# Kernel optimization log

Hardware: AMD Instinct MI355X
Metric: run time of the kernel (lower is better)

## Reference

```python
import jax, jax.numpy as jnp
import numpy as np

S, NB, C = 7, 2, 20
LAMBDA_COORD, LAMBDA_NOOBJ = 5.0, 0.5
EPS = 1e-6


def _iou(a, b):
    """Midpoint-format IoU. a, b: [..., 4] = (x, y, w, h)."""
    ax1, ay1 = a[..., 0] - a[..., 2] / 2, a[..., 1] - a[..., 3] / 2
    ax2, ay2 = a[..., 0] + a[..., 2] / 2, a[..., 1] + a[..., 3] / 2
    bx1, by1 = b[..., 0] - b[..., 2] / 2, b[..., 1] - b[..., 3] / 2
    bx2, by2 = b[..., 0] + b[..., 2] / 2, b[..., 1] + b[..., 3] / 2
    iw = jnp.clip(jnp.minimum(ax2, bx2) - jnp.maximum(ax1, bx1), 0.0)
    ih = jnp.clip(jnp.minimum(ay2, by2) - jnp.maximum(ay1, by1), 0.0)
    inter = iw * ih
    area_a = jnp.abs((ax2 - ax1) * (ay2 - ay1))
    area_b = jnp.abs((bx2 - bx1) * (by2 - by1))
    return inter / (area_a + area_b - inter + EPS)


def setup_inputs() -> dict:
    key = jax.random.key(0)
    k1, k2, k3, k4 = jax.random.split(key, 4)
    N = 16384
    predictions = jax.random.uniform(k1, (N, S * S * (C + NB * 5)), dtype=jnp.float32)
    cls = jax.random.uniform(k2, (N, S, S, C), dtype=jnp.float32)
    box_rest = jax.random.uniform(k3, (N, S, S, 4), dtype=jnp.float32)  # y,w,h,conf
    u = jax.random.uniform(k4, (N, S, S, 2), dtype=jnp.float32)
    flag = jnp.where(u[..., 0] < 0.3, 1.0, u[..., 1] * 0.99)
    targets = jnp.concatenate([cls, flag[..., None], box_rest], axis=-1)  # [N,S,S,25]
    return {"predictions": predictions, "targets": targets}


def reference(predictions, targets):
    N = predictions.shape[0]
    pred = predictions.reshape(N, S, S, C + NB * 5)
    class_pred = pred[..., :C]                      # [N,S,S,20]
    b1 = pred[..., C:C + 5]                         # [N,S,S,5]
    b2 = pred[..., C + 5:C + 10]                    # [N,S,S,5]
    tbox = targets[..., C:C + 5]                    # [N,S,S,5]
    obj = (targets[..., C] == 1.0).astype(pred.dtype)  # [N,S,S]

    iou1 = _iou(b1[..., :4], tbox[..., :4])
    iou2 = _iou(b2[..., :4], tbox[..., :4])
    resp = jnp.where((iou1 > iou2)[..., None], b1, b2)  # responsible box [N,S,S,5]

    xy = (resp[..., 0] - tbox[..., 0]) ** 2 + (resp[..., 1] - tbox[..., 1]) ** 2
    wh = (jnp.sqrt(resp[..., 2]) - jnp.sqrt(tbox[..., 2])) ** 2 \
       + (jnp.sqrt(resp[..., 3]) - jnp.sqrt(tbox[..., 3])) ** 2
    coord = LAMBDA_COORD * (xy + wh)
    conf = (resp[..., 4] - tbox[..., 4]) ** 2
    cls_loss = jnp.sum((class_pred - targets[..., :C]) ** 2, axis=-1)

    obj_terms = jnp.sum(obj * (coord + conf + cls_loss))
    noobj_terms = LAMBDA_NOOBJ * jnp.sum((1.0 - obj) * (b1[..., 4] ** 2 + b2[..., 4] ** 2))
    return (obj_terms + noobj_terms) / N
```

## Files before the change

### kernel.cpp

```cpp
#include <hip/hip_runtime.h>
#include <math.h>

#define SS 7
#define CC 20
#define CELL_PRED 30
#define CELL_TGT  25
#define BLOCK 64

__device__ __forceinline__ float iou_box(const float* __restrict__ a,
                                         const float* __restrict__ b) {
    const float EPS = 1e-6f;
    float ax1 = a[0] - a[2] * 0.5f, ay1 = a[1] - a[3] * 0.5f;
    float ax2 = a[0] + a[2] * 0.5f, ay2 = a[1] + a[3] * 0.5f;
    float bx1 = b[0] - b[2] * 0.5f, by1 = b[1] - b[3] * 0.5f;
    float bx2 = b[0] + b[2] * 0.5f, by2 = b[1] + b[3] * 0.5f;
    float iw = fmaxf(fminf(ax2, bx2) - fmaxf(ax1, bx1), 0.0f);
    float ih = fmaxf(fminf(ay2, by2) - fmaxf(ay1, by1), 0.0f);
    float inter = iw * ih;
    float area_a = fabsf((ax2 - ax1) * (ay2 - ay1));
    float area_b = fabsf((bx2 - bx1) * (by2 - by1));
    return inter / (area_a + area_b - inter + EPS);
}

__global__ __launch_bounds__(BLOCK) void yolo_cell_loss(
    const float* __restrict__ pred,
    const float* __restrict__ tgt,
    float* __restrict__ partials,
    int nCells)
{
    __shared__ __align__(16) float s_pred[BLOCK * CELL_PRED];
    __shared__ __align__(16) float s_tgt [BLOCK * CELL_TGT];

    const int tid = threadIdx.x;
    const int blockCell = blockIdx.x * BLOCK;
    const bool fullBlock = (blockCell + BLOCK) <= nCells;

    if (fullBlock) {
        const float4* gp = (const float4*)(pred + (size_t)blockCell * CELL_PRED);
        float4* sp = (float4*)s_pred;
        #pragma unroll
        for (int i = tid; i < BLOCK * CELL_PRED / 4; i += BLOCK) sp[i] = gp[i];
        const float4* gt = (const float4*)(tgt + (size_t)blockCell * CELL_TGT);
        float4* st = (float4*)s_tgt;
        #pragma unroll
        for (int i = tid; i < BLOCK * CELL_TGT / 4; i += BLOCK) st[i] = gt[i];
    } else {
        int nc = nCells - blockCell;
        if (nc < 0) nc = 0;
        for (int i = tid; i < nc * CELL_PRED; i += BLOCK)
            s_pred[i] = pred[(size_t)blockCell * CELL_PRED + i];
        for (int i = tid; i < nc * CELL_TGT; i += BLOCK)
            s_tgt[i] = tgt[(size_t)blockCell * CELL_TGT + i];
    }
    __syncthreads();

    float loss = 0.0f;
    const int cell = blockCell + tid;
    if (cell < nCells) {
        const float* p = s_pred + tid * CELL_PRED;
        const float* t = s_tgt  + tid * CELL_TGT;

        const float* b1 = p + CC;
        const float* b2 = p + CC + 5;
        const float* tb = t + CC;

        float obj = (tb[0] == 1.0f) ? 1.0f : 0.0f;

        float iou1 = iou_box(b1, tb);
        float iou2 = iou_box(b2, tb);
        bool pick1 = iou1 > iou2;
        float r0 = pick1 ? b1[0] : b2[0];
        float r1 = pick1 ? b1[1] : b2[1];
        float r2 = pick1 ? b1[2] : b2[2];
        float r3 = pick1 ? b1[3] : b2[3];
        float r4 = pick1 ? b1[4] : b2[4];

        float dx = r0 - tb[0], dy = r1 - tb[1];
        float xy = dx * dx + dy * dy;
        float dw = sqrtf(r2) - sqrtf(tb[2]);
        float dh = sqrtf(r3) - sqrtf(tb[3]);
        float wh = dw * dw + dh * dh;
        float coord = 5.0f * (xy + wh);
        float dconf = r4 - tb[4];
        float conf = dconf * dconf;

        float cls = 0.0f;
        #pragma unroll
        for (int k = 0; k < CC; ++k) {
            float d = p[k] - t[k];
            cls += d * d;
        }

        float noobj = 0.5f * (1.0f - obj) * (b1[4] * b1[4] + b2[4] * b2[4]);
        loss = obj * (coord + conf + cls) + noobj;
    }

    #pragma unroll
    for (int off = 32; off > 0; off >>= 1)
        loss += __shfl_down(loss, off, 64);
    if (tid == 0) partials[blockIdx.x] = loss;
}

__global__ __launch_bounds__(256) void yolo_final_reduce(
    const float* __restrict__ partials, int nPartials, double invN,
    float* __restrict__ out)
{
    __shared__ double s_red[4];
    double sum = 0.0;
    const float4* p4 = (const float4*)partials;
    int n4 = nPartials >> 2;
    for (int i = threadIdx.x; i < n4; i += 256) {
        float4 v = p4[i];
        sum += (double)v.x + (double)v.y + (double)v.z + (double)v.w;
    }
    for (int i = (n4 << 2) + threadIdx.x; i < nPartials; i += 256)
        sum += (double)partials[i];
    #pragma unroll
    for (int off = 32; off > 0; off >>= 1)
        sum += __shfl_down(sum, off, 64);
    if ((threadIdx.x & 63) == 0) s_red[threadIdx.x >> 6] = sum;
    __syncthreads();
    if (threadIdx.x == 0) {
        double s = s_red[0] + s_red[1] + s_red[2] + s_red[3];
        out[0] = (float)(s * invN);
    }
}

extern "C" void kernel_launch(void* const* d_in, const int* in_sizes, int n_in,
                              void* d_out, int out_size, void* d_ws, size_t ws_size,
                              hipStream_t stream) {
    const float* pred = (const float*)d_in[0];
    const float* tgt  = (const float*)d_in[1];
    float* out = (float*)d_out;
    float* partials = (float*)d_ws;

    const int N = in_sizes[0] / (SS * SS * CELL_PRED);
    const int nCells = N * SS * SS;
    const int nBlocks = (nCells + BLOCK - 1) / BLOCK;

    yolo_cell_loss<<<nBlocks, BLOCK, 0, stream>>>(pred, tgt, partials, nCells);
    yolo_final_reduce<<<1, 256, 0, stream>>>(partials, nBlocks, 1.0 / (double)N, out);
}
```

Measured before the change: 207.2 us.

## Replace shared-memory staging with grid-stride direct per-thread loads

Drops the LDS staging of each block's cells. Each thread now reads its own cell's prediction (as float2) and target values straight from global memory inside a grid-stride loop over a fixed grid of 1024 blocks of 256 threads, with a two-level shuffle plus shared-memory block reduction. This removes the __syncthreads barrier and LDS traffic and cuts the partials array to 1024 entries. The cost is uncoalesced strided per-thread loads (120-byte and 100-byte strides), which lean on the cache to merge accesses and may use bandwidth less efficiently than the old coalesced float4 staging.

```diff
diff --git a/kernel.cpp b/kernel.cpp
--- a/kernel.cpp
+++ b/kernel.cpp
@@ -5,115 +5,118 @@
 #define CC 20
 #define CELL_PRED 30
 #define CELL_TGT  25
-#define BLOCK 64
+#define BLOCK 256
+#define GRID 1024
 
-__device__ __forceinline__ float iou_box(const float* __restrict__ a,
-                                         const float* __restrict__ b) {
+__device__ __forceinline__ float cell_loss(const float* __restrict__ pred,
+                                           const float* __restrict__ tgt,
+                                           int c) {
     const float EPS = 1e-6f;
-    float ax1 = a[0] - a[2] * 0.5f, ay1 = a[1] - a[3] * 0.5f;
-    float ax2 = a[0] + a[2] * 0.5f, ay2 = a[1] + a[3] * 0.5f;
-    float bx1 = b[0] - b[2] * 0.5f, by1 = b[1] - b[3] * 0.5f;
-    float bx2 = b[0] + b[2] * 0.5f, by2 = b[1] + b[3] * 0.5f;
-    float iw = fmaxf(fminf(ax2, bx2) - fmaxf(ax1, bx1), 0.0f);
-    float ih = fmaxf(fminf(ay2, by2) - fmaxf(ay1, by1), 0.0f);
-    float inter = iw * ih;
-    float area_a = fabsf((ax2 - ax1) * (ay2 - ay1));
-    float area_b = fabsf((bx2 - bx1) * (by2 - by1));
-    return inter / (area_a + area_b - inter + EPS);
+    const float* tp = tgt + (size_t)c * CELL_TGT;
+    float tv[CELL_TGT];
+    #pragma unroll
+    for (int j = 0; j < CELL_TGT; ++j) tv[j] = tp[j];
+
+    const float2* p2 = (const float2*)(pred + (size_t)c * CELL_PRED);
+    float cls = 0.0f;
+    #pragma unroll
+    for (int j = 0; j < 10; ++j) {
+        float2 v = p2[j];
+        float d0 = v.x - tv[2 * j];
+        float d1 = v.y - tv[2 * j + 1];
+        cls += d0 * d0;
+        cls += d1 * d1;
+    }
+    float b[10];
+    #pragma unroll
+    for (int j = 0; j < 5; ++j) {
+        float2 v = p2[10 + j];
+        b[2 * j] = v.x; b[2 * j + 1] = v.y;
+    }
+    const float* b1 = b;
+    const float* b2 = b + 5;
+    const float* tb = tv + CC;
+
+    float obj = (tb[0] == 1.0f) ? 1.0f : 0.0f;
+
+    float t_x1 = tb[0] - tb[2] * 0.5f, t_y1 = tb[1] - tb[3] * 0.5f;
+    float t_x2 = tb[0] + tb[2] * 0.5f, t_y2 = tb[1] + tb[3] * 0.5f;
+    float t_area = fabsf((t_x2 - t_x1) * (t_y2 - t_y1));
+
+    float a_x1 = b1[0] - b1[2] * 0.5f, a_y1 = b1[1] - b1[3] * 0.5f;
+    float a_x2 = b1[0] + b1[2] * 0.5f, a_y2 = b1[1] + b1[3] * 0.5f;
+    float iw1 = fmaxf(fminf(a_x2, t_x2) - fmaxf(a_x1, t_x1), 0.0f);
+    float ih1 = fmaxf(fminf(a_y2, t_y2) - fmaxf(a_y1, t_y1), 0.0f);
+    float inter1 = iw1 * ih1;
+    float area1 = fabsf((a_x2 - a_x1) * (a_y2 - a_y1));
+    float iou1 = inter1 / (area1 + t_area - inter1 + EPS);
+
+    float c_x1 = b2[0] - b2[2] * 0.5f, c_y1 = b2[1] - b2[3] * 0.5f;
+    float c_x2 = b2[0] + b2[2] * 0.5f, c_y2 = b2[1] + b2[3] * 0.5f;
+    float iw2 = fmaxf(fminf(c_x2, t_x2) - fmaxf(c_x1, t_x1), 0.0f);
+    float ih2 = fmaxf(fminf(c_y2, t_y2) - fmaxf(c_y1, t_y1), 0.0f);
+    float inter2 = iw2 * ih2;
+    float area2 = fabsf((c_x2 - c_x1) * (c_y2 - c_y1));
+    float iou2 = inter2 / (area2 + t_area - inter2 + EPS);
+
+    bool pick1 = iou1 > iou2;
+    float r0 = pick1 ? b1[0] : b2[0];
+    float r1 = pick1 ? b1[1] : b2[1];
+    float r2 = pick1 ? b1[2] : b2[2];
+    float r3 = pick1 ? b1[3] : b2[3];
+    float r4 = pick1 ? b1[4] : b2[4];
+
+    float dx = r0 - tb[0], dy = r1 - tb[1];
+    float xy = dx * dx + dy * dy;
+    float dw = sqrtf(r2) - sqrtf(tb[2]);
+    float dh = sqrtf(r3) - sqrtf(tb[3]);
+    float wh = dw * dw + dh * dh;
+    float coord = 5.0f * (xy + wh);
+    float dconf = r4 - tb[4];
+    float conf = dconf * dconf;
+
+    float noobj = 0.5f * (1.0f - obj) * (b1[4] * b1[4] + b2[4] * b2[4]);
+    return obj * (coord + conf + cls) + noobj;
 }
 
-__global__ __launch_bounds__(BLOCK) void yolo_cell_loss(
+__global__ __launch_bounds__(BLOCK) void yolo_stream(
     const float* __restrict__ pred,
     const float* __restrict__ tgt,
     float* __restrict__ partials,
-    int nCells)
+    int nCells, int fullIters)
 {
-    __shared__ __align__(16) float s_pred[BLOCK * CELL_PRED];
-    __shared__ __align__(16) float s_tgt [BLOCK * CELL_TGT];
-
     const int tid = threadIdx.x;
-    const int blockCell = blockIdx.x * BLOCK;
-    const bool fullBlock = (blockCell + BLOCK) <= nCells;
-
-    if (fullBlock) {
-        const float4* gp = (const float4*)(pred + (size_t)blockCell * CELL_PRED);
-        float4* sp = (float4*)s_pred;
-        #pragma unroll
-        for (int i = tid; i < BLOCK * CELL_PRED / 4; i += BLOCK) sp[i] = gp[i];
-        const float4* gt = (const float4*)(tgt + (size_t)blockCell * CELL_TGT);
-        float4* st = (float4*)s_tgt;
-        #pragma unroll
-        for (int i = tid; i < BLOCK * CELL_TGT / 4; i += BLOCK) st[i] = gt[i];
-    } else {
-        int nc = nCells - blockCell;
-        if (nc < 0) nc = 0;
-        for (int i = tid; i < nc * CELL_PRED; i += BLOCK)
-            s_pred[i] = pred[(size_t)blockCell * CELL_PRED + i];
-        for (int i = tid; i < nc * CELL_TGT; i += BLOCK)
-            s_tgt[i] = tgt[(size_t)blockCell * CELL_TGT + i];
-    }
-    __syncthreads();
+    int c = blockIdx.x * BLOCK + tid;
+    const int stride = GRID * BLOCK;
 
     float loss = 0.0f;
-    const int cell = blockCell + tid;
-    if (cell < nCells) {
-        const float* p = s_pred + tid * CELL_PRED;
-        const float* t = s_tgt  + tid * CELL_TGT;
-
-        const float* b1 = p + CC;
-        const float* b2 = p + CC + 5;
-        const float* tb = t + CC;
-
-        float obj = (tb[0] == 1.0f) ? 1.0f : 0.0f;
-
-        float iou1 = iou_box(b1, tb);
-        float iou2 = iou_box(b2, tb);
-        bool pick1 = iou1 > iou2;
-        float r0 = pick1 ? b1[0] : b2[0];
-        float r1 = pick1 ? b1[1] : b2[1];
-        float r2 = pick1 ? b1[2] : b2[2];
-        float r3 = pick1 ? b1[3] : b2[3];
-        float r4 = pick1 ? b1[4] : b2[4];
-
-        float dx = r0 - tb[0], dy = r1 - tb[1];
-        float xy = dx * dx + dy * dy;
-        float dw = sqrtf(r2) - sqrtf(tb[2]);
-        float dh = sqrtf(r3) - sqrtf(tb[3]);
-        float wh = dw * dw + dh * dh;
-        float coord = 5.0f * (xy + wh);
-        float dconf = r4 - tb[4];
-        float conf = dconf * dconf;
-
-        float cls = 0.0f;
-        #pragma unroll
-        for (int k = 0; k < CC; ++k) {
-            float d = p[k] - t[k];
-            cls += d * d;
-        }
-
-        float noobj = 0.5f * (1.0f - obj) * (b1[4] * b1[4] + b2[4] * b2[4]);
-        loss = obj * (coord + conf + cls) + noobj;
-    }
+    for (int it = 0; it < fullIters; ++it, c += stride)
+        loss += cell_loss(pred, tgt, c);
+    if (c < nCells)
+        loss += cell_loss(pred, tgt, c);
 
     #pragma unroll
     for (int off = 32; off > 0; off >>= 1)
         loss += __shfl_down(loss, off, 64);
-    if (tid == 0) partials[blockIdx.x] = loss;
+    __shared__ float s_red[4];
+    if ((tid & 63) == 0) s_red[tid >> 6] = loss;
+    __syncthreads();
+    if (tid == 0)
+        partials[blockIdx.x] = (s_red[0] + s_red[1]) + (s_red[2] + s_red[3]);
 }
 
-__global__ __launch_bounds__(256) void yolo_final_reduce(
+__global__ __launch_bounds__(BLOCK) void yolo_final_reduce(
     const float* __restrict__ partials, int nPartials, double invN,
     float* __restrict__ out)
 {
     __shared__ double s_red[4];
+    const float4* p4 = (const float4*)partials;
     double sum = 0.0;
-    const float4* p4 = (const float4*)partials;
-    int n4 = nPartials >> 2;
-    for (int i = threadIdx.x; i < n4; i += 256) {
+    for (int i = threadIdx.x; i < (nPartials >> 2); i += BLOCK) {
         float4 v = p4[i];
         sum += (double)v.x + (double)v.y + (double)v.z + (double)v.w;
     }
-    for (int i = (n4 << 2) + threadIdx.x; i < nPartials; i += 256)
+    for (int i = ((nPartials >> 2) << 2) + threadIdx.x; i < nPartials; i += BLOCK)
         sum += (double)partials[i];
     #pragma unroll
     for (int off = 32; off > 0; off >>= 1)
@@ -121,7 +124,7 @@
     if ((threadIdx.x & 63) == 0) s_red[threadIdx.x >> 6] = sum;
     __syncthreads();
     if (threadIdx.x == 0) {
-        double s = s_red[0] + s_red[1] + s_red[2] + s_red[3];
+        double s = (s_red[0] + s_red[1]) + (s_red[2] + s_red[3]);
         out[0] = (float)(s * invN);
     }
 }
@@ -136,8 +139,9 @@
 
     const int N = in_sizes[0] / (SS * SS * CELL_PRED);
     const int nCells = N * SS * SS;
-    const int nBlocks = (nCells + BLOCK - 1) / BLOCK;
+    const int stride = GRID * BLOCK;
+    const int fullIters = nCells / stride;
 
-    yolo_cell_loss<<<nBlocks, BLOCK, 0, stream>>>(pred, tgt, partials, nCells);
-    yolo_final_reduce<<<1, 256, 0, stream>>>(partials, nBlocks, 1.0 / (double)N, out);
+    yolo_stream<<<GRID, BLOCK, 0, stream>>>(pred, tgt, partials, nCells, fullIters);
+    yolo_final_reduce<<<1, BLOCK, 0, stream>>>(partials, GRID, 1.0 / (double)N, out);
 }
```

Result: faster. 198.3 us (-4.3%).
